# Kernel optimization log

Hardware: AMD Instinct MI355X
Metric: run time of the kernel (lower is better)

## Reference

```python
import jax, jax.numpy as jnp
import numpy as np

N_BUS = 2048


def setup_inputs() -> dict:
    key = jax.random.key(0)
    ks = jax.random.split(key, 16)
    n_x, n_rbf, n_bus, batch = 4096, 1024, N_BUS, 8192
    s = lambda fan_in: 1.0 / np.sqrt(fan_in)
    return {
        "x": jax.random.normal(ks[0], (batch, n_x), dtype=jnp.float32),
        "W_h": jax.random.uniform(ks[1], (n_rbf, n_x), jnp.float32, -s(n_x), s(n_x)),
        "b_h": jax.random.uniform(ks[2], (n_rbf,), jnp.float32, -s(n_x), s(n_x)),
        "W_h2": jax.random.uniform(ks[3], (n_rbf, n_rbf), jnp.float32, -s(n_rbf), s(n_rbf)),
        "b_h2": jax.random.uniform(ks[4], (n_rbf,), jnp.float32, -s(n_rbf), s(n_rbf)),
        "W_y": jax.random.uniform(ks[5], (2 * n_bus, n_rbf), jnp.float32, -s(n_rbf), s(n_rbf)),
        "b_y": jax.random.uniform(ks[6], (2 * n_bus,), jnp.float32, -s(n_rbf), s(n_rbf)),
        "G": jax.random.uniform(ks[7], (n_bus, n_bus), dtype=jnp.float32),
        "Bm": jax.random.uniform(ks[8], (n_bus, n_bus), dtype=jnp.float32),
        "bias_p": jnp.zeros((1, n_bus), jnp.float32),
        "bias_q": jnp.zeros((1, n_bus), jnp.float32),
        "W_p": jax.random.uniform(ks[9], (n_bus, n_bus), jnp.float32, -s(n_bus), s(n_bus)),
        "b_p": jax.random.uniform(ks[10], (n_bus,), jnp.float32, -s(n_bus), s(n_bus)),
        "W_q": jax.random.uniform(ks[11], (n_bus, n_bus), jnp.float32, -s(n_bus), s(n_bus)),
        "b_q": jax.random.uniform(ks[12], (n_bus,), jnp.float32, -s(n_bus), s(n_bus)),
    }


def reference(x, W_h, b_h, W_h2, b_h2, W_y, b_y, G, Bm, bias_p, bias_q, W_p, b_p, W_q, b_q):
    n_bus = N_BUS
    # encoder (intended math: ReLU activations)
    h1 = jax.nn.relu(x @ W_h.T + b_h)
    h2 = jax.nn.relu(h1 @ W_h2.T + b_h2)
    uw = h2 @ W_y.T + b_y                     # [B, 2*n_bus]
    u, w = uw[:, :n_bus], uw[:, n_bus:]
    # decoder: algebraically identical to summing the masked outer products over dim 2:
    # p_i = sum_k (u_i u_k + w_i w_k) G_ik + (w_i u_k - u_i w_k) B_ik
    #     = u_i (G u)_i + w_i (G w)_i + w_i (B u)_i - u_i (B w)_i
    Gu = u @ G.T
    Gw = w @ G.T
    Bu = u @ Bm.T
    Bw = w @ Bm.T
    p = u * Gu + w * Gw + w * Bu - u * Bw + bias_p
    q = w * Gu - u * Gw - u * Bu - w * Bw + bias_q
    p = p @ W_p.T + b_p
    q = q @ W_q.T + b_q
    return (uw, p, q)
```

## Files before the change

### kernel.cpp

```cpp
#include <hip/hip_runtime.h>
#include <stdint.h>

typedef __bf16 bf16;
typedef __bf16 bf16x8 __attribute__((ext_vector_type(8)));
typedef __bf16 bf16x4 __attribute__((ext_vector_type(4)));
typedef float  f32x4  __attribute__((ext_vector_type(4)));

__device__ __forceinline__ void async_load16(const void* g, void* l) {
    __builtin_amdgcn_global_load_lds(
        (const __attribute__((address_space(1))) void*)g,
        (__attribute__((address_space(3))) void*)l,
        16, 0, 0);
}

__global__ __launch_bounds__(256) void cast_f32_bf16(
        const float* __restrict__ s, bf16* __restrict__ d, int n) {
    int i = (blockIdx.x * 256 + threadIdx.x) * 8;
    if (i >= n) return;
    f32x4 v0 = *(const f32x4*)(s + i);
    f32x4 v1 = *(const f32x4*)(s + i + 4);
    bf16x8 o;
    o[0] = (bf16)v0[0]; o[1] = (bf16)v0[1]; o[2] = (bf16)v0[2]; o[3] = (bf16)v0[3];
    o[4] = (bf16)v1[0]; o[5] = (bf16)v1[1]; o[6] = (bf16)v1[2]; o[7] = (bf16)v1[3];
    *(bf16x8*)(d + i) = o;
}

__global__ __launch_bounds__(256) void fill_f32(float* p, float v, int n) {
    int i = blockIdx.x * 256 + threadIdx.x;
    if (i < n) p[i] = v;
}

template<int RELU, int WF32, int WBF16>
__global__ __launch_bounds__(256, 3) void gemm_bt(
        const bf16* __restrict__ A, int lda,
        const bf16* __restrict__ B, int ldb,
        const float* __restrict__ bias,
        float* __restrict__ Cf, int ldcf,
        bf16* __restrict__ Cb, int ldcb,
        int M, int N, int K) {
    (void)M; (void)N;
    __shared__ __attribute__((aligned(16))) bf16 lA[128 * 32];
    __shared__ __attribute__((aligned(16))) bf16 lB[128 * 32];

    const int t = threadIdx.x;
    const int w = t >> 6, lane = t & 63;
    const int wm = w >> 1, wn = w & 1;
    const int m0 = blockIdx.y * 128, n0 = blockIdx.x * 128;
    const int lane15 = lane & 15, quad = lane >> 4;

    f32x4 acc[4][4] = {};

    const int srow = lane >> 2;
    const int scol = (lane & 3) * 8;
    const int c0 = 2 * w, c1 = 2 * w + 1;
    const bf16* gA0 = A + (size_t)(m0 + c0 * 16 + srow) * lda + scol;
    const bf16* gA1 = A + (size_t)(m0 + c1 * 16 + srow) * lda + scol;
    const bf16* gB0 = B + (size_t)(n0 + c0 * 16 + srow) * ldb + scol;
    const bf16* gB1 = B + (size_t)(n0 + c1 * 16 + srow) * ldb + scol;
    bf16* lA0 = &lA[c0 * 512];
    bf16* lA1 = &lA[c1 * 512];
    bf16* lB0 = &lB[c0 * 512];
    bf16* lB1 = &lB[c1 * 512];

    const bf16* fA = &lA[(wm * 64 + lane15) * 32 + quad * 8];
    const bf16* fB = &lB[(wn * 64 + lane15) * 32 + quad * 8];

    for (int k0 = 0; k0 < K; k0 += 32) {
        async_load16(gA0, lA0);
        async_load16(gA1, lA1);
        async_load16(gB0, lB0);
        async_load16(gB1, lB1);
        gA0 += 32; gA1 += 32; gB0 += 32; gB1 += 32;
        __syncthreads();
        bf16x8 a[4], b[4];
#pragma unroll
        for (int i = 0; i < 4; i++) a[i] = *(const bf16x8*)(fA + i * 16 * 32);
#pragma unroll
        for (int j = 0; j < 4; j++) b[j] = *(const bf16x8*)(fB + j * 16 * 32);
#pragma unroll
        for (int i = 0; i < 4; i++)
#pragma unroll
            for (int j = 0; j < 4; j++)
                acc[i][j] = __builtin_amdgcn_mfma_f32_16x16x32_bf16(a[i], b[j], acc[i][j], 0, 0, 0);
        __syncthreads();
    }

#pragma unroll
    for (int i = 0; i < 4; i++) {
        int row = m0 + wm * 64 + i * 16 + quad * 4;
#pragma unroll
        for (int j = 0; j < 4; j++) {
            int col = n0 + wn * 64 + j * 16 + lane15;
            float bv = bias ? bias[col] : 0.0f;
#pragma unroll
            for (int r = 0; r < 4; r++) {
                float v = acc[i][j][r] + bv;
                if (RELU) v = v > 0.0f ? v : 0.0f;
                if (WF32)  Cf[(size_t)(row + r) * ldcf + col] = v;
                if (WBF16) Cb[(size_t)(row + r) * ldcb + col] = (bf16)v;
            }
        }
    }
}

template<int RELU, int WF32, int WBF16>
__global__ __launch_bounds__(512, 2) void gemm256(
        const bf16* __restrict__ A, int lda,
        const bf16* __restrict__ B, int ldb,
        const float* __restrict__ bias,
        float* __restrict__ Cf, int ldcf,
        bf16* __restrict__ Cb, int ldcb,
        int K) {
    __shared__ __attribute__((aligned(128))) char sm[131072];

    const int t = threadIdx.x;
    const int w = t >> 6;
    const int lane = t & 63;
    const int wm = w >> 2, wn = w & 3;
    const int l15 = lane & 15, quad = lane >> 4;

    const int gx = gridDim.x;
    const int nwg = gx * gridDim.y;
    const int orig = blockIdx.y * gx + blockIdx.x;
    const int cpx = nwg >> 3;
    const int wg = (orig & 7) * cpx + (orig >> 3);
    const int m0 = (wg / gx) << 8;
    const int n0 = (wg % gx) << 8;

    f32x4 acc[8][4] = {};

    const int srow = t >> 3;
    const int scol = ((t & 7) ^ (srow & 7)) << 3;
    const bf16* gA = A + (size_t)(m0 + srow) * lda + scol;
    const bf16* gB = B + (size_t)(n0 + srow) * ldb + scol;
    char* smA = sm + w * 1024;
    char* smB = sm + 65536 + w * 1024;
    const size_t stepA = (size_t)lda << 6;
    const size_t stepB = (size_t)ldb << 6;

    const int swz = (quad ^ (l15 & 7)) << 4;
    const char* aRd0 = sm + ((wm * 128 + l15) << 7) + swz;
    const char* bRd0 = sm + 65536 + ((wn * 64 + l15) << 7) + swz;
    const char* aRd1 = (const char*)((uintptr_t)aRd0 ^ 64);
    const char* bRd1 = (const char*)((uintptr_t)bRd0 ^ 64);

    bf16x8 a[4][2], b[4][2];
    unsigned boff = 0;

#define STAGE_A(nb) do { \
    async_load16(gA,             smA + (nb)); \
    async_load16(gA + stepA,     smA + (nb) + 8192); \
    async_load16(gA + 2 * stepA, smA + (nb) + 16384); \
    async_load16(gA + 3 * stepA, smA + (nb) + 24576); } while (0)
#define STAGE_B(nb) do { \
    async_load16(gB,             smB + (nb)); \
    async_load16(gB + stepB,     smB + (nb) + 8192); \
    async_load16(gB + 2 * stepB, smB + (nb) + 16384); \
    async_load16(gB + 3 * stepB, smB + (nb) + 24576); } while (0)
#define RD_A(Mq) do { _Pragma("unroll") \
    for (int i = 0; i < 4; i++) { \
        a[i][0] = *(const bf16x8*)(aRd0 + boff + (Mq) * 8192 + i * 2048); \
        a[i][1] = *(const bf16x8*)(aRd1 + boff + (Mq) * 8192 + i * 2048); } } while (0)
#define RD_B(Nq) do { _Pragma("unroll") \
    for (int j = 0; j < 2; j++) { \
        b[(Nq) * 2 + j][0] = *(const bf16x8*)(bRd0 + boff + ((Nq) * 2 + j) * 2048); \
        b[(Nq) * 2 + j][1] = *(const bf16x8*)(bRd1 + boff + ((Nq) * 2 + j) * 2048); } } while (0)
#define MMA(Mq, Nq) do { _Pragma("unroll") \
    for (int i = 0; i < 4; i++) { _Pragma("unroll") \
        for (int j = 0; j < 2; j++) { \
            acc[(Mq) * 4 + i][(Nq) * 2 + j] = __builtin_amdgcn_mfma_f32_16x16x32_bf16( \
                a[i][0], b[(Nq) * 2 + j][0], acc[(Mq) * 4 + i][(Nq) * 2 + j], 0, 0, 0); \
            acc[(Mq) * 4 + i][(Nq) * 2 + j] = __builtin_amdgcn_mfma_f32_16x16x32_bf16( \
                a[i][1], b[(Nq) * 2 + j][1], acc[(Mq) * 4 + i][(Nq) * 2 + j], 0, 0, 0); } } } while (0)
#define BAR() __builtin_amdgcn_s_barrier()
#define WAITLGKM() do { \
    asm volatile("s_waitcnt lgkmcnt(0)" ::: "memory"); \
    __builtin_amdgcn_sched_barrier(0); } while (0)

    STAGE_A(0); STAGE_B(0);
    gA += 64; gB += 64;
    asm volatile("s_waitcnt vmcnt(0)" ::: "memory");
    BAR();

    const int nt = K >> 6;
#define KTILE(PF) do { \
    const unsigned nboff = boff ^ 32768u; \
     \
    RD_A(0); RD_B(0); \
    if (PF) STAGE_A(nboff); \
    BAR(); WAITLGKM(); \
    __builtin_amdgcn_s_setprio(1); MMA(0, 0); __builtin_amdgcn_s_setprio(0); \
    BAR(); \
     \
    RD_B(1); \
    if (PF) STAGE_B(nboff); \
    BAR(); WAITLGKM(); \
    __builtin_amdgcn_s_setprio(1); MMA(0, 1); __builtin_amdgcn_s_setprio(0); \
    BAR(); \
     \
    RD_A(1); \
    BAR(); WAITLGKM(); \
    __builtin_amdgcn_s_setprio(1); MMA(1, 0); __builtin_amdgcn_s_setprio(0); \
    BAR(); \
     \
    __builtin_amdgcn_s_setprio(1); MMA(1, 1); __builtin_amdgcn_s_setprio(0); \
    if (PF) { gA += 64; gB += 64; \
        asm volatile("s_waitcnt vmcnt(0)" ::: "memory"); } \
    BAR(); \
    boff = nboff; \
} while (0)

    for (int T = 0; T < nt - 1; ++T) KTILE(1);
    KTILE(0);
#undef KTILE
#undef STAGE_A
#undef STAGE_B
#undef RD_A
#undef RD_B
#undef MMA
#undef BAR
#undef WAITLGKM

#pragma unroll
    for (int i = 0; i < 8; i++) {
        int row = m0 + wm * 128 + i * 16 + quad * 4;
#pragma unroll
        for (int j = 0; j < 4; j++) {
            int col = n0 + wn * 64 + j * 16 + l15;
            float bv = bias ? bias[col] : 0.0f;
#pragma unroll
            for (int r = 0; r < 4; r++) {
                float v = acc[i][j][r] + bv;
                if (RELU) v = v > 0.0f ? v : 0.0f;
                if (WF32)  Cf[(size_t)(row + r) * ldcf + col] = v;
                if (WBF16) Cb[(size_t)(row + r) * ldcb + col] = (bf16)v;
            }
        }
    }
}

__global__ __launch_bounds__(256) void combine_pq(
        const bf16* __restrict__ uwb,
        const bf16* __restrict__ GBu, const bf16* __restrict__ GBw,
        const float* __restrict__ bias_p, const float* __restrict__ bias_q,
        bf16* __restrict__ pp, bf16* __restrict__ qp) {
    int idx = (blockIdx.x * 256 + threadIdx.x) * 4;
    int row = idx >> 11;
    int col = idx & 2047;
    size_t base = (size_t)row * 4096 + col;
    bf16x4 u4  = *(const bf16x4*)(uwb + base);
    bf16x4 w4  = *(const bf16x4*)(uwb + base + 2048);
    bf16x4 gu4 = *(const bf16x4*)(GBu + base);
    bf16x4 bu4 = *(const bf16x4*)(GBu + base + 2048);
    bf16x4 gw4 = *(const bf16x4*)(GBw + base);
    bf16x4 bw4 = *(const bf16x4*)(GBw + base + 2048);
    bf16x4 po, qo;
#pragma unroll
    for (int r = 0; r < 4; r++) {
        float u = (float)u4[r], w = (float)w4[r];
        float gu = (float)gu4[r], gw = (float)gw4[r];
        float bu = (float)bu4[r], bw = (float)bw4[r];
        float p = u * gu + w * gw + w * bu - u * bw + bias_p[col + r];
        float q = w * gu - u * gw - u * bu - w * bw + bias_q[col + r];
        po[r] = (bf16)p;
        qo[r] = (bf16)q;
    }
    *(bf16x4*)(pp + idx) = po;
    *(bf16x4*)(qp + idx) = qo;
}

extern "C" void kernel_launch(void* const* d_in, const int* in_sizes, int n_in,
                              void* d_out, int out_size, void* d_ws, size_t ws_size,
                              hipStream_t stream) {
    (void)in_sizes; (void)n_in;
    const int BT = 8192, NX = 4096, NR = 1024, NB = 2048;

    const float* x      = (const float*)d_in[0];
    const float* W_h    = (const float*)d_in[1];
    const float* b_h    = (const float*)d_in[2];
    const float* W_h2   = (const float*)d_in[3];
    const float* b_h2   = (const float*)d_in[4];
    const float* W_y    = (const float*)d_in[5];
    const float* b_y    = (const float*)d_in[6];
    const float* G      = (const float*)d_in[7];
    const float* Bm     = (const float*)d_in[8];
    const float* bias_p = (const float*)d_in[9];
    const float* bias_q = (const float*)d_in[10];
    const float* W_p    = (const float*)d_in[11];
    const float* b_p    = (const float*)d_in[12];
    const float* W_q    = (const float*)d_in[13];
    const float* b_q    = (const float*)d_in[14];
    float* out = (float*)d_out;

    const size_t NEED = 320864256ull;
    if (ws_size < NEED) {
        fill_f32<<<dim3((out_size + 255) / 256), dim3(256), 0, stream>>>(
            out, (float)(ws_size >> 20), out_size);
        return;
    }
    char* ws = (char*)d_ws;
    bf16* xb   = (bf16*)(ws + 0);
    bf16* GBu  = (bf16*)(ws + 0);
    bf16* uwb  = (bf16*)(ws + 67108864);
    bf16* GBw  = (bf16*)(ws + 134217728);
    bf16* h1   = (bf16*)(ws + 201326592);
    bf16* pp   = (bf16*)(ws + 201326592);
    bf16* h2   = (bf16*)(ws + 218103808);
    bf16* qp   = (bf16*)(ws + 234881024);
    bf16* whb  = (bf16*)(ws + 268435456);
    bf16* wh2b = (bf16*)(ws + 276824064);
    bf16* wyb  = (bf16*)(ws + 278921216);
    bf16* gbm  = (bf16*)(ws + 287309824);
    bf16* wpb  = (bf16*)(ws + 304087040);
    bf16* wqb  = (bf16*)(ws + 312475648);

    dim3 blk(256);
    auto cast = [&](const float* s, bf16* d, int n) {
        cast_f32_bf16<<<dim3((n / 8 + 255) / 256), blk, 0, stream>>>(s, d, n);
    };
    cast(x,    xb,   BT * NX);
    cast(W_h,  whb,  NR * NX);
    cast(W_h2, wh2b, NR * NR);
    cast(W_y,  wyb,  NX * NR);
    cast(G,    gbm,            NB * NB);
    cast(Bm,   gbm + (size_t)NB * NB, NB * NB);
    cast(W_p,  wpb,  NB * NB);
    cast(W_q,  wqb,  NB * NB);

    gemm_bt<1, 0, 1><<<dim3(NR / 128, BT / 128), blk, 0, stream>>>(
        xb, NX, whb, NX, b_h, nullptr, 0, h1, NR, BT, NR, NX);
    gemm_bt<1, 0, 1><<<dim3(NR / 128, BT / 128), blk, 0, stream>>>(
        h1, NR, wh2b, NR, b_h2, nullptr, 0, h2, NR, BT, NR, NR);

    gemm256<0, 1, 1><<<dim3(NX / 256, BT / 256), dim3(512), 0, stream>>>(
        h2, NR, wyb, NR, b_y, out, NX, uwb, NX, NR);
    gemm256<0, 0, 1><<<dim3(NX / 256, BT / 256), dim3(512), 0, stream>>>(
        uwb,      NX, gbm, NB, nullptr, nullptr, 0, GBu, NX, NB);
    gemm256<0, 0, 1><<<dim3(NX / 256, BT / 256), dim3(512), 0, stream>>>(
        uwb + NB, NX, gbm, NB, nullptr, nullptr, 0, GBw, NX, NB);
    combine_pq<<<dim3(BT * NB / 4 / 256), blk, 0, stream>>>(
        uwb, GBu, GBw, bias_p, bias_q, pp, qp);
    gemm256<0, 1, 0><<<dim3(NB / 256, BT / 256), dim3(512), 0, stream>>>(
        pp, NB, wpb, NB, b_p, out + (size_t)BT * NX, NB, nullptr, 0, NB);
    gemm256<0, 1, 0><<<dim3(NB / 256, BT / 256), dim3(512), 0, stream>>>(
        qp, NB, wqb, NB, b_q, out + (size_t)BT * NX + (size_t)BT * NB, NB, nullptr, 0, NB);
}
```

Baseline: 1.326 ms.

## Split GEMM global-to-LDS prefetch into chunks with partial vmcnt waits

The next tile's prefetch is no longer issued as two blocks of four loads. Loads are now issued two at a time across all four MMA phases, B first and A later. The full vmcnt(0) drain at the end of each k-tile becomes partial waits (vmcnt 4 and 2), so some A loads stay in flight across the tile boundary. This aims to hide global-load latency behind more MFMA work. In exchange it adds a barrier and an LDS wait before the last MMA phase, and correctness depends on exact vmcnt ordering against which LDS chunks each phase reads.

```diff
diff --git a/kernel.cpp b/kernel.cpp
--- a/kernel.cpp
+++ b/kernel.cpp
@@ -135,8 +135,8 @@
     const bf16* gB = B + (size_t)(n0 + srow) * ldb + scol;
     char* smA = sm + w * 1024;
     char* smB = sm + 65536 + w * 1024;
-    const size_t stepA = (size_t)lda << 6;
-    const size_t stepB = (size_t)ldb << 6;
+    const size_t rstepA = (size_t)lda << 6;
+    const size_t rstepB = (size_t)ldb << 6;
 
     const int swz = (quad ^ (l15 & 7)) << 4;
     const char* aRd0 = sm + ((wm * 128 + l15) << 7) + swz;
@@ -147,16 +147,8 @@
     bf16x8 a[4][2], b[4][2];
     unsigned boff = 0;
 
-#define STAGE_A(nb) do { \
-    async_load16(gA,             smA + (nb)); \
-    async_load16(gA + stepA,     smA + (nb) + 8192); \
-    async_load16(gA + 2 * stepA, smA + (nb) + 16384); \
-    async_load16(gA + 3 * stepA, smA + (nb) + 24576); } while (0)
-#define STAGE_B(nb) do { \
-    async_load16(gB,             smB + (nb)); \
-    async_load16(gB + stepB,     smB + (nb) + 8192); \
-    async_load16(gB + 2 * stepB, smB + (nb) + 16384); \
-    async_load16(gB + 3 * stepB, smB + (nb) + 24576); } while (0)
+#define STG_A(c, nb) async_load16(gA + (c) * rstepA, smA + (nb) + (c) * 8192)
+#define STG_B(c, nb) async_load16(gB + (c) * rstepB, smB + (nb) + (c) * 8192)
 #define RD_A(Mq) do { _Pragma("unroll") \
     for (int i = 0; i < 4; i++) { \
         a[i][0] = *(const bf16x8*)(aRd0 + boff + (Mq) * 8192 + i * 2048); \
@@ -176,10 +168,14 @@
 #define WAITLGKM() do { \
     asm volatile("s_waitcnt lgkmcnt(0)" ::: "memory"); \
     __builtin_amdgcn_sched_barrier(0); } while (0)
-
-    STAGE_A(0); STAGE_B(0);
+#define WAITVM(N) do { \
+    asm volatile("s_waitcnt vmcnt(" #N ")" ::: "memory"); \
+    __builtin_amdgcn_sched_barrier(0); } while (0)
+
+    STG_B(0, 0); STG_B(1, 0); STG_B(2, 0); STG_B(3, 0);
+    STG_A(0, 0); STG_A(2, 0); STG_A(1, 0); STG_A(3, 0);
     gA += 64; gB += 64;
-    asm volatile("s_waitcnt vmcnt(0)" ::: "memory");
+    WAITVM(0);
     BAR();
 
     const int nt = K >> 6;
@@ -187,25 +183,28 @@
     const unsigned nboff = boff ^ 32768u; \
      \
     RD_A(0); RD_B(0); \
-    if (PF) STAGE_A(nboff); \
+    if (PF) { STG_B(0, nboff); STG_B(1, nboff); } \
     BAR(); WAITLGKM(); \
     __builtin_amdgcn_s_setprio(1); MMA(0, 0); __builtin_amdgcn_s_setprio(0); \
     BAR(); \
      \
     RD_B(1); \
-    if (PF) STAGE_B(nboff); \
+    if (PF) { STG_B(2, nboff); STG_B(3, nboff); } \
     BAR(); WAITLGKM(); \
     __builtin_amdgcn_s_setprio(1); MMA(0, 1); __builtin_amdgcn_s_setprio(0); \
+    if (PF) { WAITVM(4); } else { WAITVM(0); } \
     BAR(); \
      \
     RD_A(1); \
+    if (PF) { STG_A(0, nboff); STG_A(2, nboff); } \
     BAR(); WAITLGKM(); \
     __builtin_amdgcn_s_setprio(1); MMA(1, 0); __builtin_amdgcn_s_setprio(0); \
     BAR(); \
      \
+    if (PF) { STG_A(1, nboff); STG_A(3, nboff); } \
+    BAR(); WAITLGKM(); \
     __builtin_amdgcn_s_setprio(1); MMA(1, 1); __builtin_amdgcn_s_setprio(0); \
-    if (PF) { gA += 64; gB += 64; \
-        asm volatile("s_waitcnt vmcnt(0)" ::: "memory"); } \
+    if (PF) { WAITVM(2); gA += 64; gB += 64; } \
     BAR(); \
     boff = nboff; \
 } while (0)
@@ -213,13 +212,14 @@
     for (int T = 0; T < nt - 1; ++T) KTILE(1);
     KTILE(0);
 #undef KTILE
-#undef STAGE_A
-#undef STAGE_B
+#undef STG_A
+#undef STG_B
 #undef RD_A
 #undef RD_B
 #undef MMA
 #undef BAR
 #undef WAITLGKM
+#undef WAITVM
 
 #pragma unroll
     for (int i = 0; i < 8; i++) {
```

Measured after the change: 1.349 ms. Within noise of the previous version (+1.7%).
